# Optimization experiments

Measured on AMD Instinct MI355X. Metric: run time of the kernel, lower is better.

Reference implementation:

```python
import jax, jax.numpy as jnp
import numpy as np

N, C, F, NB = 256, 4, 256, 32   # batch, in_channels, in_features, neighbors
OC, OF = 4, 256                 # out_channels, out_features


def setup_inputs() -> dict:
    key = jax.random.key(0)
    k1, k2, k3 = jax.random.split(key, 3)
    x = jax.random.normal(k1, (N, C, F), dtype=jnp.float32)
    neighbor = jax.random.normal(k2, (N, NB, C, F), dtype=jnp.float32)
    # Conv1d(in=2C, out=OC*OF, kernel_size=F, bias=False) weight
    W = jax.random.normal(k3, (OC * OF, 2 * C, F), dtype=jnp.float32) * 0.02
    return {"x": x, "neighbor": neighbor, "W": W}


def _feature_adjacency(x, neighbor):
    # batched version of per-sample einsum('ca,ncb->cab')
    fadj = jnp.einsum('Nca,Nncb->Ncab', x, neighbor)  # (N,C,F,F)
    fadj = fadj + jnp.swapaxes(fadj, -2, -1)
    # sign-sqrt
    s = jnp.sign(fadj) * jnp.sqrt(jnp.clip(jnp.abs(fadj), 1e-8, None))
    # row(col)-normalize over dim -2, then NaN mask
    adj = s / (jnp.abs(s).sum(-2, keepdims=True) + 1e-7)
    return jnp.where(jnp.isnan(adj), 0.0, adj)


def reference(x, neighbor, W):
    adj = _feature_adjacency(x, neighbor)            # (N,C,F,F)
    ax = jnp.einsum('Ncab,Ncb->Nca', adj, x)         # adj @ x
    xcat = jnp.concatenate([ax, x], axis=1)          # (N,2C,F)
    # Conv1d with kernel_size=F over length-F input == flat contraction
    out = jnp.einsum('Nif,oif->No', xcat, W).reshape(x.shape[0], OC, OF)
    return (out, adj)
```

## Files before the change

### kernel.cpp

```cpp
#include <hip/hip_runtime.h>
#include <math.h>

namespace {
constexpr int N_ = 256, C_ = 4, F_ = 256, NB_ = 32;
constexpr int O_ = 1024;
constexpr int OUT_ELEMS = N_ * O_;
typedef float f32x4 __attribute__((ext_vector_type(4)));
}

__global__ __launch_bounds__(256) void adj_kernel(
    const float* __restrict__ x,
    const float* __restrict__ neighbor,
    float* __restrict__ adj,
    float* __restrict__ ax_out)
{
  __shared__ float x_l[F_], s_l[F_], w_l[F_];
  __shared__ float red[4][F_];
  const int blk = blockIdx.x;
  const int n = blk >> 2, c = blk & 3;
  const int t = threadIdx.x;
  const int rs = t >> 6;
  const int lane = t & 63;
  const int b0 = lane * 4;

  const int base = (n * C_ + c) * F_;
  x_l[t] = x[base + t];
  {
    const float* p = neighbor + ((size_t)(n * NB_) * C_ + c) * F_ + t;
    float s = 0.f;
    #pragma unroll
    for (int j = 0; j < NB_; ++j) s += p[(size_t)j * C_ * F_];
    s_l[t] = s;
  }
  __syncthreads();

  const float4 xb4 = *(const float4*)&x_l[b0];
  const float4 sb4 = *(const float4*)&s_l[b0];
  const float xbv[4] = {xb4.x, xb4.y, xb4.z, xb4.w};
  const float sbv[4] = {sb4.x, sb4.y, sb4.z, sb4.w};

  float cs[4] = {0.f, 0.f, 0.f, 0.f};
  const int a0r = rs * 64;
  #pragma unroll 4
  for (int a = a0r; a < a0r + 64; ++a) {
    const float xa = x_l[a], sa = s_l[a];
    #pragma unroll
    for (int j = 0; j < 4; ++j) {
      float v = fmaf(xa, sbv[j], xbv[j] * sa);
      float r = __builtin_amdgcn_sqrtf(fmaxf(fabsf(v), 1e-8f));
      cs[j] += (v != 0.f) ? r : 0.f;
    }
  }
  *(float4*)&red[rs][b0] = make_float4(cs[0], cs[1], cs[2], cs[3]);
  __syncthreads();

  float invv[4];
  {
    const float4 r0 = *(const float4*)&red[0][b0];
    const float4 r1 = *(const float4*)&red[1][b0];
    const float4 r2 = *(const float4*)&red[2][b0];
    const float4 r3 = *(const float4*)&red[3][b0];
    invv[0] = 1.f / (r0.x + r1.x + r2.x + r3.x + 1e-7f);
    invv[1] = 1.f / (r0.y + r1.y + r2.y + r3.y + 1e-7f);
    invv[2] = 1.f / (r0.z + r1.z + r2.z + r3.z + 1e-7f);
    invv[3] = 1.f / (r0.w + r1.w + r2.w + r3.w + 1e-7f);
  }
  if (rs == 0) {
    *(float4*)&w_l[b0] = make_float4(invv[0] * xbv[0], invv[1] * xbv[1],
                                     invv[2] * xbv[2], invv[3] * xbv[3]);
  }
  __syncthreads();

  float axp[4] = {0.f, 0.f, 0.f, 0.f};
  float* arow = adj + (size_t)(n * C_ + c) * (F_ * F_);
  #pragma unroll 2
  for (int a = a0r; a < a0r + 64; ++a) {
    const float xa = x_l[a], sa = s_l[a], wa = w_l[a];
    float o[4];
    #pragma unroll
    for (int j = 0; j < 4; ++j) {
      float v = fmaf(xa, sbv[j], xbv[j] * sa);
      float r = __builtin_amdgcn_sqrtf(fmaxf(fabsf(v), 1e-8f));
      float tt = (v != 0.f) ? copysignf(r, v) : 0.f;
      o[j] = tt * invv[j];
      axp[j] = fmaf(tt, wa, axp[j]);
    }
    f32x4 ov = {o[0], o[1], o[2], o[3]};
    __builtin_nontemporal_store(ov, (f32x4*)&arow[(size_t)a * F_ + b0]);
  }
  *(float4*)&red[rs][b0] = make_float4(axp[0], axp[1], axp[2], axp[3]);
  __syncthreads();
  if (rs == 0) {
    const float4 r0 = *(const float4*)&red[0][b0];
    const float4 r1 = *(const float4*)&red[1][b0];
    const float4 r2 = *(const float4*)&red[2][b0];
    const float4 r3 = *(const float4*)&red[3][b0];
    const float4 axv = make_float4(r0.x + r1.x + r2.x + r3.x,
                                   r0.y + r1.y + r2.y + r3.y,
                                   r0.z + r1.z + r2.z + r3.z,
                                   r0.w + r1.w + r2.w + r3.w);
    *(float4*)&ax_out[base + b0] = axv;
  }
}

__global__ __launch_bounds__(256) void gemm_kernel(
    const float* __restrict__ ax,
    const float* __restrict__ x,
    const float* __restrict__ W,
    float* __restrict__ out)
{
  __shared__ float As[32][64];
  __shared__ float Bs[32][64];
  const int tid = threadIdx.x;
  const int m0 = blockIdx.x * 64, o0 = blockIdx.y * 64;
  const int mi = tid >> 4, oi = tid & 15;
  const int r = tid >> 2, kq = (tid & 3) * 8;
  float acc[4][4] = {};

  const int kbeg = blockIdx.z * 256;
  for (int k0 = kbeg; k0 < kbeg + 256; k0 += 32) {
    const float* Ab = (k0 < 1024) ? ax + k0 : x + (k0 - 1024);
    const float4 a0 = *(const float4*)&Ab[(size_t)(m0 + r) * 1024 + kq];
    const float4 a1 = *(const float4*)&Ab[(size_t)(m0 + r) * 1024 + kq + 4];
    const float4 b0 = *(const float4*)&W[(size_t)(o0 + r) * 2048 + k0 + kq];
    const float4 b1 = *(const float4*)&W[(size_t)(o0 + r) * 2048 + k0 + kq + 4];
    __syncthreads();
    As[kq + 0][r] = a0.x; As[kq + 1][r] = a0.y;
    As[kq + 2][r] = a0.z; As[kq + 3][r] = a0.w;
    As[kq + 4][r] = a1.x; As[kq + 5][r] = a1.y;
    As[kq + 6][r] = a1.z; As[kq + 7][r] = a1.w;
    Bs[kq + 0][r] = b0.x; Bs[kq + 1][r] = b0.y;
    Bs[kq + 2][r] = b0.z; Bs[kq + 3][r] = b0.w;
    Bs[kq + 4][r] = b1.x; Bs[kq + 5][r] = b1.y;
    Bs[kq + 6][r] = b1.z; Bs[kq + 7][r] = b1.w;
    __syncthreads();
    #pragma unroll
    for (int kk = 0; kk < 32; ++kk) {
      const float4 av = *(const float4*)&As[kk][mi * 4];
      const float4 bv = *(const float4*)&Bs[kk][oi * 4];
      const float am[4] = {av.x, av.y, av.z, av.w};
      const float bm[4] = {bv.x, bv.y, bv.z, bv.w};
      #pragma unroll
      for (int i = 0; i < 4; ++i)
        #pragma unroll
        for (int j = 0; j < 4; ++j)
          acc[i][j] = fmaf(am[i], bm[j], acc[i][j]);
    }
  }
  #pragma unroll
  for (int i = 0; i < 4; ++i)
    #pragma unroll
    for (int j = 0; j < 4; ++j)
      atomicAdd(&out[(size_t)(m0 + mi * 4 + i) * 1024 + o0 + oi * 4 + j],
                acc[i][j]);
}

extern "C" void kernel_launch(void* const* d_in, const int* in_sizes, int n_in,
                              void* d_out, int out_size, void* d_ws,
                              size_t ws_size, hipStream_t stream) {
  const float* x = (const float*)d_in[0];
  const float* neighbor = (const float*)d_in[1];
  const float* W = (const float*)d_in[2];
  float* out = (float*)d_out;
  float* adj = out + OUT_ELEMS;
  float* ax = (float*)d_ws;

  (void)hipMemsetAsync(out, 0, OUT_ELEMS * sizeof(float), stream);
  adj_kernel<<<dim3(N_ * C_), dim3(256), 0, stream>>>(x, neighbor, adj, ax);
  gemm_kernel<<<dim3(256 / 64, O_ / 64, 8), dim3(256), 0, stream>>>(ax, x, W,
                                                                    out);
}
```

Before: 347.1 us.

## Retile GEMM to 128x128 with register prefetch and use rsq in adjacency kernel

The GEMM moves from 64x64 tiles with 4x4 per-thread outputs to 128x128 tiles with 8x8 outputs and a 16-way split-K. It adds register prefetch of the next K slab and a padded, swizzled shared-memory layout, aiming for more arithmetic per load and to hide global latency. The adjacency kernel packs x, s and w into one float4 shared array and replaces sqrt plus select with rsq times v. This drops the copysign and zero branch but depends on the 1e-8 clamp for near-zero values. More split-K slices mean more atomic adds, and the larger accumulator array raises register pressure.

```diff
diff --git a/kernel.cpp b/kernel.cpp
--- a/kernel.cpp
+++ b/kernel.cpp
@@ -14,7 +14,7 @@
     float* __restrict__ adj,
     float* __restrict__ ax_out)
 {
-  __shared__ float x_l[F_], s_l[F_], w_l[F_];
+  __shared__ float4 xsw[F_];
   __shared__ float red[4][F_];
   const int blk = blockIdx.x;
   const int n = blk >> 2, c = blk & 3;
@@ -24,31 +24,36 @@
   const int b0 = lane * 4;
 
   const int base = (n * C_ + c) * F_;
-  x_l[t] = x[base + t];
   {
+    const float xv = x[base + t];
     const float* p = neighbor + ((size_t)(n * NB_) * C_ + c) * F_ + t;
     float s = 0.f;
     #pragma unroll
     for (int j = 0; j < NB_; ++j) s += p[(size_t)j * C_ * F_];
-    s_l[t] = s;
-  }
-  __syncthreads();
-
-  const float4 xb4 = *(const float4*)&x_l[b0];
-  const float4 sb4 = *(const float4*)&s_l[b0];
-  const float xbv[4] = {xb4.x, xb4.y, xb4.z, xb4.w};
-  const float sbv[4] = {sb4.x, sb4.y, sb4.z, sb4.w};
+    xsw[t] = make_float4(xv, s, 0.f, 0.f);
+  }
+  __syncthreads();
+
+  float xbv[4], sbv[4];
+  #pragma unroll
+  for (int j = 0; j < 4; ++j) {
+    const float4 q = xsw[b0 + j];
+    xbv[j] = q.x;
+    sbv[j] = q.y;
+  }
 
   float cs[4] = {0.f, 0.f, 0.f, 0.f};
   const int a0r = rs * 64;
   #pragma unroll 4
   for (int a = a0r; a < a0r + 64; ++a) {
-    const float xa = x_l[a], sa = s_l[a];
+    const float2 xs = *(const float2*)&xsw[a];
+    const float xa = xs.x, sa = xs.y;
     #pragma unroll
     for (int j = 0; j < 4; ++j) {
       float v = fmaf(xa, sbv[j], xbv[j] * sa);
-      float r = __builtin_amdgcn_sqrtf(fmaxf(fabsf(v), 1e-8f));
-      cs[j] += (v != 0.f) ? r : 0.f;
+      float m = fmaxf(fabsf(v), 1e-8f);
+      float rq = __builtin_amdgcn_rsqf(m);
+      cs[j] = fmaf(fabsf(v), rq, cs[j]);
     }
   }
   *(float4*)&red[rs][b0] = make_float4(cs[0], cs[1], cs[2], cs[3]);
@@ -66,22 +71,24 @@
     invv[3] = 1.f / (r0.w + r1.w + r2.w + r3.w + 1e-7f);
   }
   if (rs == 0) {
-    *(float4*)&w_l[b0] = make_float4(invv[0] * xbv[0], invv[1] * xbv[1],
-                                     invv[2] * xbv[2], invv[3] * xbv[3]);
+    #pragma unroll
+    for (int j = 0; j < 4; ++j) xsw[b0 + j].z = invv[j] * xbv[j];
   }
   __syncthreads();
 
   float axp[4] = {0.f, 0.f, 0.f, 0.f};
   float* arow = adj + (size_t)(n * C_ + c) * (F_ * F_);
-  #pragma unroll 2
+  #pragma unroll 4
   for (int a = a0r; a < a0r + 64; ++a) {
-    const float xa = x_l[a], sa = s_l[a], wa = w_l[a];
+    const float4 q = xsw[a];
+    const float xa = q.x, sa = q.y, wa = q.z;
     float o[4];
     #pragma unroll
     for (int j = 0; j < 4; ++j) {
       float v = fmaf(xa, sbv[j], xbv[j] * sa);
-      float r = __builtin_amdgcn_sqrtf(fmaxf(fabsf(v), 1e-8f));
-      float tt = (v != 0.f) ? copysignf(r, v) : 0.f;
+      float m = fmaxf(fabsf(v), 1e-8f);
+      float rq = __builtin_amdgcn_rsqf(m);
+      float tt = v * rq;
       o[j] = tt * invv[j];
       axp[j] = fmaf(tt, wa, axp[j]);
     }
@@ -103,56 +110,84 @@
   }
 }
 
+namespace {
+constexpr int TM = 128, TO = 128, BK = 32, PL = 144;
+__device__ __forceinline__ int swz(int c) { return c + ((c >> 5) << 2); }
+}
+
 __global__ __launch_bounds__(256) void gemm_kernel(
     const float* __restrict__ ax,
     const float* __restrict__ x,
     const float* __restrict__ W,
     float* __restrict__ out)
 {
-  __shared__ float As[32][64];
-  __shared__ float Bs[32][64];
+  __shared__ float As[BK * PL];
+  __shared__ float Bs[BK * PL];
   const int tid = threadIdx.x;
-  const int m0 = blockIdx.x * 64, o0 = blockIdx.y * 64;
+  const int m0 = blockIdx.x * TM, o0 = blockIdx.y * TO;
+  const int kbeg = blockIdx.z * 128;
+  const float* Ab = (kbeg < 1024) ? ax + kbeg : x + (kbeg - 1024);
+
+  const int sr = tid >> 1;
+  const int kq = (tid & 1) * 16;
+  const int psr = swz(sr);
   const int mi = tid >> 4, oi = tid & 15;
-  const int r = tid >> 2, kq = (tid & 3) * 8;
-  float acc[4][4] = {};
-
-  const int kbeg = blockIdx.z * 256;
-  for (int k0 = kbeg; k0 < kbeg + 256; k0 += 32) {
-    const float* Ab = (k0 < 1024) ? ax + k0 : x + (k0 - 1024);
-    const float4 a0 = *(const float4*)&Ab[(size_t)(m0 + r) * 1024 + kq];
-    const float4 a1 = *(const float4*)&Ab[(size_t)(m0 + r) * 1024 + kq + 4];
-    const float4 b0 = *(const float4*)&W[(size_t)(o0 + r) * 2048 + k0 + kq];
-    const float4 b1 = *(const float4*)&W[(size_t)(o0 + r) * 2048 + k0 + kq + 4];
+  const int pa = swz(mi * 8), pb = swz(oi * 8);
+
+  const float* Arow = Ab + (size_t)(m0 + sr) * 1024 + kq;
+  const float* Brow = W + (size_t)(o0 + sr) * 2048 + kbeg + kq;
+
+  float4 ra[4], rb[4];
+  #pragma unroll
+  for (int q = 0; q < 4; ++q) {
+    ra[q] = *(const float4*)&Arow[q * 4];
+    rb[q] = *(const float4*)&Brow[q * 4];
+  }
+
+  float acc[8][8] = {};
+
+  for (int tt = 0; tt < 4; ++tt) {
+    #pragma unroll
+    for (int q = 0; q < 4; ++q) {
+      const float av[4] = {ra[q].x, ra[q].y, ra[q].z, ra[q].w};
+      const float bv[4] = {rb[q].x, rb[q].y, rb[q].z, rb[q].w};
+      #pragma unroll
+      for (int e = 0; e < 4; ++e) {
+        As[(kq + q * 4 + e) * PL + psr] = av[e];
+        Bs[(kq + q * 4 + e) * PL + psr] = bv[e];
+      }
+    }
     __syncthreads();
-    As[kq + 0][r] = a0.x; As[kq + 1][r] = a0.y;
-    As[kq + 2][r] = a0.z; As[kq + 3][r] = a0.w;
-    As[kq + 4][r] = a1.x; As[kq + 5][r] = a1.y;
-    As[kq + 6][r] = a1.z; As[kq + 7][r] = a1.w;
-    Bs[kq + 0][r] = b0.x; Bs[kq + 1][r] = b0.y;
-    Bs[kq + 2][r] = b0.z; Bs[kq + 3][r] = b0.w;
-    Bs[kq + 4][r] = b1.x; Bs[kq + 5][r] = b1.y;
-    Bs[kq + 6][r] = b1.z; Bs[kq + 7][r] = b1.w;
+    if (tt < 3) {
+      #pragma unroll
+      for (int q = 0; q < 4; ++q) {
+        ra[q] = *(const float4*)&Arow[(tt + 1) * BK + q * 4];
+        rb[q] = *(const float4*)&Brow[(tt + 1) * BK + q * 4];
+      }
+    }
+    #pragma unroll 8
+    for (int kk = 0; kk < BK; ++kk) {
+      const float4 a0 = *(const float4*)&As[kk * PL + pa];
+      const float4 a1 = *(const float4*)&As[kk * PL + pa + 4];
+      const float4 b0 = *(const float4*)&Bs[kk * PL + pb];
+      const float4 b1 = *(const float4*)&Bs[kk * PL + pb + 4];
+      const float am[8] = {a0.x, a0.y, a0.z, a0.w, a1.x, a1.y, a1.z, a1.w};
+      const float bm[8] = {b0.x, b0.y, b0.z, b0.w, b1.x, b1.y, b1.z, b1.w};
+      #pragma unroll
+      for (int i = 0; i < 8; ++i)
+        #pragma unroll
+        for (int j = 0; j < 8; ++j)
+          acc[i][j] = fmaf(am[i], bm[j], acc[i][j]);
+    }
     __syncthreads();
-    #pragma unroll
-    for (int kk = 0; kk < 32; ++kk) {
-      const float4 av = *(const float4*)&As[kk][mi * 4];
-      const float4 bv = *(const float4*)&Bs[kk][oi * 4];
-      const float am[4] = {av.x, av.y, av.z, av.w};
-      const float bm[4] = {bv.x, bv.y, bv.z, bv.w};
-      #pragma unroll
-      for (int i = 0; i < 4; ++i)
-        #pragma unroll
-        for (int j = 0; j < 4; ++j)
-          acc[i][j] = fmaf(am[i], bm[j], acc[i][j]);
-    }
-  }
+  }
+
   #pragma unroll
-  for (int i = 0; i < 4; ++i)
-    #pragma unroll
-    for (int j = 0; j < 4; ++j)
-      atomicAdd(&out[(size_t)(m0 + mi * 4 + i) * 1024 + o0 + oi * 4 + j],
-                acc[i][j]);
+  for (int i = 0; i < 8; ++i) {
+    float* orow = &out[(size_t)(m0 + mi * 8 + i) * 1024 + o0 + oi * 8];
+    #pragma unroll
+    for (int j = 0; j < 8; ++j) atomicAdd(&orow[j], acc[i][j]);
+  }
 }
 
 extern "C" void kernel_launch(void* const* d_in, const int* in_sizes, int n_in,
@@ -167,6 +202,6 @@
 
   (void)hipMemsetAsync(out, 0, OUT_ELEMS * sizeof(float), stream);
   adj_kernel<<<dim3(N_ * C_), dim3(256), 0, stream>>>(x, neighbor, adj, ax);
-  gemm_kernel<<<dim3(256 / 64, O_ / 64, 8), dim3(256), 0, stream>>>(ax, x, W,
-                                                                    out);
-}
+  gemm_kernel<<<dim3(256 / TM, O_ / TO, 16), dim3(256), 0, stream>>>(ax, x, W,
+                                                                     out);
+}
```

Measured after the change: 560.8 us. 61.6% more time.
